# Optimization experiments

Measured on AMD Instinct MI355X. Metric: run time of the kernel, lower is better.

Reference implementation:

```python
import jax, jax.numpy as jnp
import numpy as np
from jax import lax

BS, K, N = 8, 8, 16            # batch, gathers per sample, picks per curve
T, WG = 3072, 64               # gather time samples, traces
H, WC = 256, 256               # CVEncoder ScaleSize
RH, RW = 1024, 512             # resize (also GatherEncoder outLen=RH)
T0, T1 = 0.0, 7000.0           # tInt[0], tInt[-1]


def setup_inputs() -> dict:
    key = jax.random.key(0)
    ks = jax.random.split(key, 8)
    gather = jax.random.normal(ks[0], (BS, K, T, WG), jnp.float32)
    # cv: times sorted, strictly > 0, within [T0, T1]; velocities within VMM range
    times = jnp.sort(jax.random.uniform(ks[1], (BS, K, N), minval=100.0, maxval=T1), axis=-1)
    vels = jnp.sort(jax.random.uniform(ks[2], (BS, K, N), minval=1500.0, maxval=4500.0), axis=-1)
    cv = jnp.stack([times, vels], axis=-1).astype(jnp.float32)
    VMM = jnp.tile(jnp.array([1500.0, 4500.0], jnp.float32), (BS, 1))
    def cw(k, shape):
        return (jax.random.normal(k, shape, jnp.float32) * 0.1)
    params = dict(
        w1=cw(ks[3], (1, 1, 3, 3)), b1=jnp.zeros((1,), jnp.float32), g1=jnp.ones((1,), jnp.float32), be1=jnp.zeros((1,), jnp.float32),
        w2=cw(ks[4], (2, 3, 3, 3)), b2=jnp.zeros((2,), jnp.float32), g2=jnp.ones((2,), jnp.float32), be2=jnp.zeros((2,), jnp.float32),
        w3=cw(ks[5], (1, 2, 3, 2)), b3=jnp.zeros((1,), jnp.float32), g3=jnp.ones((1,), jnp.float32), be3=jnp.zeros((1,), jnp.float32),
        wf=cw(ks[6], (1, 1, 3, 3)), bf=jnp.zeros((1,), jnp.float32), gf=jnp.ones((1,), jnp.float32), bef=jnp.zeros((1,), jnp.float32),
    )
    return {"gather": gather, "cv": cv, "VMM": VMM, **params}


def _conv(x, w, b, stride, pad):
    y = lax.conv_general_dilated(x, w, stride, pad, dimension_numbers=("NCHW", "OIHW", "NCHW"))
    return y + b[None, :, None, None]


def _bn(x, g, b, eps=1e-5):
    # training-mode BatchNorm2d: stats over (N, H, W)
    m = jnp.mean(x, (0, 2, 3), keepdims=True)
    v = jnp.var(x, (0, 2, 3), keepdims=True)
    return (x - m) / jnp.sqrt(v + eps) * g[None, :, None, None] + b[None, :, None, None]


def _lrelu(x):
    return jnp.where(x >= 0, x, 0.1 * x)


def _cbl(x, w, b, g, be, stride):
    return _lrelu(_bn(_conv(x, w, b, stride, "VALID"), g, be))


def _maxpool(x, k):
    p = k // 2
    return lax.reduce_window(x, -jnp.inf, lax.max, (1, 1, k, k), (1, 1, 1, 1),
                             ((0, 0), (0, 0), (p, p), (p, p)))


def _cv_mask(cv, VMM):
    # normalize times to fractional row index and velocities to fractional col index
    dt = (T1 - T0) / (H - 1)
    t_idx = (cv[..., 0] - T0) / dt                                        # (BS,K,N)
    dv = (VMM[:, 1] - VMM[:, 0]) / (WC - 1)                               # (BS,)
    v_idx = (cv[..., 1] - VMM[:, 0, None, None]) / dv[:, None, None]      # (BS,K,N)
    t_flat = t_idx.reshape(-1, N)
    v_flat = v_idx.reshape(-1, N)
    tq = jnp.arange(H, dtype=jnp.float32)
    # per-curve piecewise-linear interpolation of v over the time grid
    v_curve = jax.vmap(lambda xp, fp: jnp.interp(tq, xp, fp))(t_flat, v_flat)  # (M,H)
    v_int = jnp.clip(v_curve.astype(jnp.int32), 0, WC - 1)
    M = BS * K
    mask = jnp.full((M, H, WC), 0.01, jnp.float32)
    mask = mask.at[jnp.arange(M)[:, None], jnp.arange(H)[None, :], v_int].add(0.9)
    mask = mask.reshape(BS, K, H, WC)
    # bilinear resize, half-pixel centers == torch align_corners=False
    return jax.image.resize(mask, (BS, K, RH, RW), method="linear")


def _forward(gather, cv, VMM, w1, b1, g1, be1, w2, b2, g2, be2, w3, b3, g3, be3, wf, bf, gf, bef):
    cv_mask = lax.stop_gradient(_cv_mask(cv, VMM))          # CVEncoder runs under no_grad
    x = gather.reshape(-1, 1, T, WG)                        # (BS*K,1,T,WG)
    x = x / jnp.max(jnp.abs(x))                             # mode='mute': keep sign
    x = _cbl(x, w1, b1, g1, be1, (3, 2))                    # (M,1,1024,31)
    xcat = jnp.concatenate([x, _maxpool(x, 3), _maxpool(x, 5)], axis=1)
    x = _cbl(xcat, w2, b2, g2, be2, (3, 2))                 # (M,2,341,15)
    x = _cbl(x, w3, b3, g3, be3, (3, 2))                    # (M,1,113,7)
    x = jax.image.resize(x, (x.shape[0], 1, RH, 1), method="linear")
    genr = x.reshape(BS, K, RH, 1)
    mix = jnp.sum(genr * cv_mask, axis=1, keepdims=True)    # (BS,1,RH,RW)
    y = _conv(mix, wf, bf, (1, 1), ((1, 1), (1, 1)))
    return _lrelu(_bn(y, gf, bef))


def reference(gather, cv, VMM, w1, b1, g1, be1, w2, b2, g2, be2, w3, b3, g3, be3, wf, bf, gf, bef):
    return _forward(gather, cv, VMM, w1, b1, g1, be1, w2, b2, g2, be2, w3, b3, g3, be3, wf, bf, gf, bef)
```

## Files before the change

kernel.cpp:

```cpp
#include <hip/hip_runtime.h>
#include <math.h>

#define BSZ 8
#define KG  8
#define NP  16
#define MM  64
#define TT  3072
#define WGN 64
#define HH  256
#define WCN 256
#define RHN 1024
#define RWN 512

#define C1H 1024
#define C1W 31
#define C2H 341
#define C2W 15
#define C3H 113
#define C3W 7

#define N1 (MM*C1H*C1W)
#define N2 (MM*C2H*C2W)
#define N3 (MM*C3H*C3W)
#define NF (BSZ*RHN*RWN)

#define SL 64
__device__ __forceinline__ int stat_slot(int bid) {
    return ((bid & 7) << 3) | ((bid >> 3) & 7);
}

#define OFF_VINT 5376
#define OFF_Y1   (OFF_VINT + MM*HH*4)
#define OFF_Y2   (OFF_Y1  + N1*4)
#define OFF_Y3   (OFF_Y2  + 2*N2*4)
#define OFF_GENR (OFF_Y3  + N3*4)
#define OFF_Y5   (OFF_GENR + MM*RHN*4)

__device__ __forceinline__ void blockAdd2(double s, double ss, double* o0, double* o1) {
    __shared__ double red[4][2];
    __syncthreads();
    int lane = threadIdx.x & 63, wid = threadIdx.x >> 6;
#pragma unroll
    for (int off = 32; off > 0; off >>= 1) {
        s  += __shfl_down(s,  off, 64);
        ss += __shfl_down(ss, off, 64);
    }
    if (lane == 0) { red[wid][0] = s; red[wid][1] = ss; }
    __syncthreads();
    if (threadIdx.x == 0) {
        double a = 0, b = 0;
        int nw = blockDim.x >> 6;
        for (int i = 0; i < nw; i++) { a += red[i][0]; b += red[i][1]; }
        int slot = stat_slot(blockIdx.x);
        atomicAdd(&o0[slot], a); atomicAdd(&o1[slot], b);
    }
}

__device__ __forceinline__ float2 bn_ab(const double* __restrict__ sums, int c,
                                        const float* __restrict__ g,
                                        const float* __restrict__ be, double n) {
    double sum = 0, sumsq = 0;
#pragma unroll 8
    for (int j = 0; j < SL; j++) {
        sum   += sums[(2 * c) * SL + j];
        sumsq += sums[(2 * c + 1) * SL + j];
    }
    double mean = sum / n;
    double var  = sumsq / n - mean * mean;
    double a = (double)g[c] / sqrt(var + 1e-5);
    return make_float2((float)a, (float)((double)be[c] - mean * a));
}

#define K1_R 16
#define K1_ROWS (3*K1_R)
#define K1_CH 4
__global__ void k_conv1(const float* __restrict__ g, const float* __restrict__ w1,
                        const float* __restrict__ b1,
                        float* __restrict__ y1, double* sums) {
    __shared__ float sm[K1_ROWS * WGN];
    int m  = blockIdx.x >> 4;
    int bg = blockIdx.x & 15;
    const float4* src0 = (const float4*)(g + (size_t)m * TT * WGN
                                           + (size_t)(bg * K1_CH * K1_R * 3) * WGN);
    float w[9];
#pragma unroll
    for (int i = 0; i < 9; i++) w[i] = w1[i];
    float bb = b1[0];
    float4 ra0, ra1, ra2, rb0, rb1, rb2;
    ra0 = src0[threadIdx.x];
    ra1 = src0[threadIdx.x + 256];
    ra2 = src0[threadIdx.x + 512];
    double s = 0, ss = 0;
    float4* dst = (float4*)sm;
#pragma unroll
    for (int i = 0; i < K1_CH; i++) {
        if (i & 1) {
            dst[threadIdx.x]       = rb0;
            dst[threadIdx.x + 256] = rb1;
            dst[threadIdx.x + 512] = rb2;
        } else {
            dst[threadIdx.x]       = ra0;
            dst[threadIdx.x + 256] = ra1;
            dst[threadIdx.x + 512] = ra2;
        }
        __syncthreads();
        if (i + 1 < K1_CH) {
            const float4* srcn = src0 + (size_t)(i + 1) * 768;
            if (i & 1) {
                ra0 = srcn[threadIdx.x];
                ra1 = srcn[threadIdx.x + 256];
                ra2 = srcn[threadIdx.x + 512];
            } else {
                rb0 = srcn[threadIdx.x];
                rb1 = srcn[threadIdx.x + 256];
                rb2 = srcn[threadIdx.x + 512];
            }
        }
        int oh0 = (bg * K1_CH + i) * K1_R;
        float* yb = y1 + (size_t)m * C1H * C1W + (size_t)oh0 * C1W;
        for (int o = threadIdx.x; o < K1_R * C1W; o += 256) {
            int lo = o / C1W, ow = o % C1W;
            const float* xp = sm + (3 * lo) * WGN + ow * 2;
            float acc = bb;
#pragma unroll
            for (int r = 0; r < 3; r++)
#pragma unroll
                for (int c = 0; c < 3; c++) acc += w[r * 3 + c] * xp[r * WGN + c];
            yb[o] = acc;
            s += acc; ss += (double)acc * (double)acc;
        }
        __syncthreads();
    }
    blockAdd2(s, ss, &sums[0], &sums[SL]);
}

#define F2_OH 32
#define F2_NCH 11
#define F2_NRMAX (3*F2_OH + 4)
__global__ void k_fused2(const float* __restrict__ y1, const double* __restrict__ sums_r,
                         const float* __restrict__ g1, const float* __restrict__ be1,
                         const float* __restrict__ w2, const float* __restrict__ b2,
                         float* __restrict__ y2, double* sums) {
    __shared__ float sact[F2_NRMAX][32];
    __shared__ float sr3[F2_NRMAX][32];
    __shared__ float sr5[F2_NRMAX][32];
    float2 ab1 = bn_ab(sums_r, 0, g1, be1, (double)N1);
    int m   = blockIdx.x / F2_NCH;
    int ch  = blockIdx.x % F2_NCH;
    int oh0 = ch * F2_OH;
    int OHa = min(F2_OH, C2H - oh0);
    int NR  = 3 * OHa + 4;
    int gl0 = 3 * oh0 - 2;
    const float* yp = y1 + (size_t)m * C1H * C1W;
    for (int i = threadIdx.x; i < NR * C1W; i += blockDim.x) {
        int l = i / C1W, w = i % C1W;
        int gr = gl0 + l;
        float v = -INFINITY;
        if (gr >= 0 && gr < C1H) {
            v = ab1.x * yp[gr * C1W + w] + ab1.y;
            v = v >= 0.f ? v : 0.1f * v;
        }
        sact[l][w] = v;
    }
    __syncthreads();
    for (int i = threadIdx.x; i < NR * C1W; i += blockDim.x) {
        int l = i / C1W, w = i % C1W;
        int wl1 = max(w - 1, 0), wr1 = min(w + 1, C1W - 1);
        int wl2 = max(w - 2, 0), wr2 = min(w + 2, C1W - 1);
        float c  = sact[l][w];
        float m3 = fmaxf(fmaxf(sact[l][wl1], c), sact[l][wr1]);
        float m5 = fmaxf(fmaxf(m3, sact[l][wl2]), sact[l][wr2]);
        sr3[l][w] = m3;
        sr5[l][w] = m5;
    }
    __syncthreads();
    double s0 = 0, ss0 = 0, s1 = 0, ss1 = 0;
    for (int o = threadIdx.x; o < OHa * C2W; o += blockDim.x) {
        int lo = o / C2W, ow = o % C2W;
        float a0 = b2[0], acc1 = b2[1];
#pragma unroll
        for (int i = 0; i < 3; i++) {
            int l = 3 * lo + 2 + i;
#pragma unroll
            for (int j = 0; j < 3; j++) {
                int wc = 2 * ow + j;
                float v0 = sact[l][wc];
                float v1 = fmaxf(fmaxf(sr3[l - 1][wc], sr3[l][wc]), sr3[l + 1][wc]);
                float v2 = fmaxf(fmaxf(fmaxf(sr5[l - 2][wc], sr5[l - 1][wc]), sr5[l][wc]),
                                 fmaxf(sr5[l + 1][wc], sr5[l + 2][wc]));
                int ki = i * 3 + j;
                a0   += w2[ki] * v0 + w2[9 + ki] * v1 + w2[18 + ki] * v2;
                acc1 += w2[27 + ki] * v0 + w2[36 + ki] * v1 + w2[45 + ki] * v2;
            }
        }
        size_t ob = (size_t)m * (2 * C2H * C2W) + (size_t)(oh0 + lo) * C2W + ow;
        y2[ob] = a0;
        y2[ob + C2H * C2W] = acc1;
        s0 += a0; ss0 += (double)a0 * a0;
        s1 += acc1; ss1 += (double)acc1 * acc1;
    }
    blockAdd2(s0, ss0, &sums[2 * SL], &sums[3 * SL]);
    blockAdd2(s1, ss1, &sums[4 * SL], &sums[5 * SL]);
}

__global__ void k_conv3(const float* __restrict__ y2, const double* __restrict__ sums_r,
                        const float* __restrict__ g2, const float* __restrict__ be2,
                        const float* __restrict__ w3, const float* __restrict__ b3,
                        float* __restrict__ y3, double* sums) {
    float2 ab20 = bn_ab(sums_r + 2 * SL, 0, g2, be2, (double)N2);
    float2 ab21 = bn_ab(sums_r + 2 * SL, 1, g2, be2, (double)N2);
    double s = 0, ss = 0;
    int stride = gridDim.x * blockDim.x;
    for (int idx = blockIdx.x * blockDim.x + threadIdx.x; idx < N3; idx += stride) {
        int ow = idx % C3W;
        int t2 = idx / C3W;
        int oh = t2 % C3H;
        int m  = t2 / C3H;
        float acc = b3[0];
#pragma unroll
        for (int i = 0; i < 2; i++) {
            float aa = i ? ab21.x : ab20.x, bb = i ? ab21.y : ab20.y;
            const float* cp = y2 + (size_t)m * (2 * C2H * C2W) + (size_t)i * C2H * C2W
                              + (size_t)(oh * 3) * C2W + ow * 2;
#pragma unroll
            for (int r = 0; r < 3; r++)
#pragma unroll
                for (int c = 0; c < 2; c++) {
                    float v = aa * cp[r * C2W + c] + bb;
                    v = v >= 0.f ? v : 0.1f * v;
                    acc += w3[i * 6 + r * 2 + c] * v;
                }
        }
        y3[idx] = acc;
        s += acc; ss += (double)acc * acc;
    }
    blockAdd2(s, ss, &sums[6 * SL], &sums[7 * SL]);
}

__global__ void k_vintgenr(const float* __restrict__ cv, const float* __restrict__ VMM,
                           const float* __restrict__ y3, const double* __restrict__ sums_r,
                           const float* __restrict__ g3, const float* __restrict__ be3,
                           int* __restrict__ vint, float* __restrict__ genr) {
    __shared__ float tt[NP], vv[NP];
    __shared__ float tile[C3H * C3W];
    int m = blockIdx.x;
    int b = m >> 3;
    float2 ab3 = bn_ab(sums_r + 6 * SL, 0, g3, be3, (double)N3);
    if (threadIdx.x < NP) {
        int n = threadIdx.x;
        float t = cv[(m * NP + n) * 2 + 0];
        float v = cv[(m * NP + n) * 2 + 1];
        float dt = 7000.0f / 255.0f;
        tt[n] = t / dt;
        float vmin = VMM[b * 2], vmax = VMM[b * 2 + 1];
        float dv = (vmax - vmin) / 255.0f;
        vv[n] = (v - vmin) / dv;
    }
    for (int i = threadIdx.x; i < C3H * C3W; i += blockDim.x) {
        float v = ab3.x * y3[m * C3H * C3W + i] + ab3.y;
        tile[i] = v >= 0.f ? v : 0.1f * v;
    }
    __syncthreads();
    {
        int h = threadIdx.x;
        float x = (float)h;
        float val;
        if (x <= tt[0]) val = vv[0];
        else if (x >= tt[NP - 1]) val = vv[NP - 1];
        else {
            int i = 1;
            while (i < NP - 1 && tt[i] <= x) i++;
            float d = tt[i] - tt[i - 1];
            val = (d != 0.f) ? vv[i - 1] + (x - tt[i - 1]) / d * (vv[i] - vv[i - 1]) : vv[i];
        }
        int vi = (int)val;
        vint[m * HH + h] = max(0, min(WCN - 1, vi));
    }
    const float cw0 = 4.f / 37.f, cw1 = 5.f / 37.f, cw2 = 6.f / 37.f, cw3 = 7.f / 37.f;
    const float cw[7] = { cw0, cw1, cw2, cw3, cw2, cw1, cw0 };
    for (int i = threadIdx.x; i < RHN; i += blockDim.x) {
        float sh = (i + 0.5f) * (113.0f / 1024.0f) - 0.5f;
        float fl = floorf(sh);
        float fr = sh - fl;
        int i0 = (int)fl, i1 = i0 + 1;
        i0 = max(0, min(C3H - 1, i0));
        i1 = max(0, min(C3H - 1, i1));
        float acc = 0.f;
#pragma unroll
        for (int x = 0; x < 7; x++) {
            float v = (1.f - fr) * tile[i0 * C3W + x] + fr * tile[i1 * C3W + x];
            acc += cw[x] * v;
        }
        genr[m * RHN + i] = acc;
    }
}

#define MC_TH 16
__device__ __forceinline__ void build_mix_tile(const float* __restrict__ genr,
                                               const int* __restrict__ vint,
                                               int b, int h0,
                                               float (*tile)[RWN + 2], float* Grow) {
    for (int i = threadIdx.x; i < (MC_TH + 2) * (RWN + 2); i += blockDim.x)
        ((float*)tile)[i] = 0.f;
    if (threadIdx.x < MC_TH + 2) Grow[threadIdx.x] = 0.f;
    __syncthreads();
    if (threadIdx.x < (MC_TH + 2) * KG) {
        int r = threadIdx.x / KG, k = threadIdx.x % KG;
        int h = h0 - 1 + r;
        if (h >= 0 && h < RHN) {
            int m = b * KG + k;
            float g = genr[m * RHN + h];
            atomicAdd(&Grow[r], g);
            float sh = (h + 0.5f) * 0.25f - 0.5f;
            float fl = floorf(sh);
            float fh = sh - fl;
            int ih0 = (int)fl, ih1 = ih0 + 1;
            ih0 = max(0, min(HH - 1, ih0));
            ih1 = max(0, min(HH - 1, ih1));
            int vv[2] = { vint[m * HH + ih0], vint[m * HH + ih1] };
            float aa[2] = { 0.9f * g * (1.f - fh), 0.9f * g * fh };
#pragma unroll
            for (int t = 0; t < 2; t++) {
                int v = vv[t]; float A = aa[t];
                if (v == 0) {
                    atomicAdd(&tile[r][1 + 0], A);
                    atomicAdd(&tile[r][1 + 1], 0.75f * A);
                    atomicAdd(&tile[r][1 + 2], 0.25f * A);
                } else if (v == WCN - 1) {
                    atomicAdd(&tile[r][1 + 509], 0.25f * A);
                    atomicAdd(&tile[r][1 + 510], 0.75f * A);
                    atomicAdd(&tile[r][1 + 511], A);
                } else {
                    atomicAdd(&tile[r][1 + 2 * v - 1], 0.25f * A);
                    atomicAdd(&tile[r][1 + 2 * v],     0.75f * A);
                    atomicAdd(&tile[r][1 + 2 * v + 1], 0.75f * A);
                    atomicAdd(&tile[r][1 + 2 * v + 2], 0.25f * A);
                }
            }
        }
    }
    __syncthreads();
    for (int i = threadIdx.x; i < (MC_TH + 2) * RWN; i += blockDim.x) {
        int r = i / RWN, w = i % RWN;
        int h = h0 - 1 + r;
        if (h >= 0 && h < RHN) tile[r][w + 1] += 0.01f * Grow[r];
    }
    __syncthreads();
}

__global__ void k_mixA(const float* __restrict__ genr, const int* __restrict__ vint,
                       const float* __restrict__ wf, const float* __restrict__ bf,
                       float* __restrict__ y5, double* sums) {
    __shared__ float tile[MC_TH + 2][RWN + 2];
    __shared__ float Grow[MC_TH + 2];
    int b   = blockIdx.x / (RHN / MC_TH);
    int h0  = (blockIdx.x % (RHN / MC_TH)) * MC_TH;
    build_mix_tile(genr, vint, b, h0, tile, Grow);
    float w[9];
#pragma unroll
    for (int i = 0; i < 9; i++) w[i] = wf[i];
    float bb = bf[0];
    double s = 0, ss = 0;
    for (int o = threadIdx.x; o < MC_TH * RWN; o += blockDim.x) {
        int lr = o / RWN, x = o % RWN;
        float acc = bb;
#pragma unroll
        for (int dr = 0; dr < 3; dr++)
#pragma unroll
            for (int dc = 0; dc < 3; dc++)
                acc += w[dr * 3 + dc] * tile[lr + dr][x + dc];
        y5[((size_t)b * RHN + (h0 + lr)) * RWN + x] = acc;
        s += acc; ss += (double)acc * acc;
    }
    blockAdd2(s, ss, &sums[8 * SL], &sums[9 * SL]);
}

__global__ void k_bnf(const float* __restrict__ y5, const double* __restrict__ sums_r,
                      const float* __restrict__ gf, const float* __restrict__ bef,
                      float* __restrict__ out) {
    float2 abf = bn_ab(sums_r + 8 * SL, 0, gf, bef, (double)NF);
    int stride = gridDim.x * blockDim.x;
    const float4* src = (const float4*)y5;
    float4* dst = (float4*)out;
    for (int i = blockIdx.x * blockDim.x + threadIdx.x; i < NF / 4; i += stride) {
        float4 v = src[i];
        float a0 = abf.x * v.x + abf.y;
        float a1 = abf.x * v.y + abf.y;
        float a2 = abf.x * v.z + abf.y;
        float a3 = abf.x * v.w + abf.y;
        v.x = a0 >= 0.f ? a0 : 0.1f * a0;
        v.y = a1 >= 0.f ? a1 : 0.1f * a1;
        v.z = a2 >= 0.f ? a2 : 0.1f * a2;
        v.w = a3 >= 0.f ? a3 : 0.1f * a3;
        dst[i] = v;
    }
}

extern "C" void kernel_launch(void* const* d_in, const int* in_sizes, int n_in,
                              void* d_out, int out_size, void* d_ws, size_t ws_size,
                              hipStream_t stream) {
    const float* gather = (const float*)d_in[0];
    const float* cv     = (const float*)d_in[1];
    const float* VMM    = (const float*)d_in[2];
    const float* w1 = (const float*)d_in[3];
    const float* b1 = (const float*)d_in[4];
    const float* g1 = (const float*)d_in[5];
    const float* be1 = (const float*)d_in[6];
    const float* w2 = (const float*)d_in[7];
    const float* b2 = (const float*)d_in[8];
    const float* g2 = (const float*)d_in[9];
    const float* be2 = (const float*)d_in[10];
    const float* w3 = (const float*)d_in[11];
    const float* b3 = (const float*)d_in[12];
    const float* g3 = (const float*)d_in[13];
    const float* be3 = (const float*)d_in[14];
    const float* wf = (const float*)d_in[15];
    const float* bf = (const float*)d_in[16];
    const float* gf = (const float*)d_in[17];
    const float* bef = (const float*)d_in[18];
    float* out = (float*)d_out;

    char* ws = (char*)d_ws;
    double* sums = (double*)ws;
    int*   vint  = (int*)(ws + OFF_VINT);
    float* y1    = (float*)(ws + OFF_Y1);
    float* y2    = (float*)(ws + OFF_Y2);
    float* y3    = (float*)(ws + OFF_Y3);
    float* genr  = (float*)(ws + OFF_GENR);
    float* y5    = (float*)(ws + OFF_Y5);

    hipMemsetAsync(d_ws, 0, 10 * SL * 8, stream);

    k_conv1<<<MM * 16, 256, 0, stream>>>(gather, w1, b1, y1, sums);
    k_fused2<<<MM * F2_NCH, 256, 0, stream>>>(y1, sums, g1, be1, w2, b2, y2, sums);
    k_conv3<<<198, 256, 0, stream>>>(y2, sums, g2, be2, w3, b3, y3, sums);
    k_vintgenr<<<MM, 256, 0, stream>>>(cv, VMM, y3, sums, g3, be3, vint, genr);
    k_mixA<<<BSZ * (RHN / MC_TH), 256, 0, stream>>>(genr, vint, wf, bf, y5, sums);
    k_bnf<<<2048, 256, 0, stream>>>(y5, sums, gf, bef, out);
}
```

Measured before the change: 184.4 us.

## Fuse vint/genr stage into neighbors and replace atomic BN stats with partial stores

Removes the separate vint/genr kernel by computing velocity indices in spare conv1 blocks and recomputing the resized, normalized genr values inline when building the mix tile. BatchNorm statistics are now written as per-block partials and reduced by one wave in the consumer kernel, replacing slot atomics and the workspace memset. Grid sizes are fixed so each thread handles a fixed number of elements. This trades one launch and a memset for redundant genr recomputation across mix blocks.

```diff
diff --git a/kernel.cpp b/kernel.cpp
--- a/kernel.cpp
+++ b/kernel.cpp
@@ -24,19 +24,40 @@
 #define N3 (MM*C3H*C3W)
 #define NF (BSZ*RHN*RWN)
 
-#define SL 64
-__device__ __forceinline__ int stat_slot(int bid) {
-    return ((bid & 7) << 3) | ((bid >> 3) & 7);
-}
-
-#define OFF_VINT 5376
+#define G1 1024
+#define G2 704
+#define G3 256
+#define G5 512
+#define G6 512
+
+#define P1S   0
+#define P1SS  1024
+#define P2S0  2048
+#define P2SS0 2752
+#define P2S1  3456
+#define P2SS1 4160
+#define P3S   4864
+#define P3SS  5120
+#define PFS   5376
+#define PFSS  5888
+
+#define OFF_VINT 51200
 #define OFF_Y1   (OFF_VINT + MM*HH*4)
 #define OFF_Y2   (OFF_Y1  + N1*4)
 #define OFF_Y3   (OFF_Y2  + 2*N2*4)
-#define OFF_GENR (OFF_Y3  + N3*4)
-#define OFF_Y5   (OFF_GENR + MM*RHN*4)
-
-__device__ __forceinline__ void blockAdd2(double s, double ss, double* o0, double* o1) {
+#define OFF_Y5   (OFF_Y3  + N3*4)
+
+#define K1_R 16
+#define K1_ROWS (3*K1_R)
+#define K1_CH 4
+#define F2_OH 32
+#define F2_NCH 11
+#define F2_NRMAX (3*F2_OH + 4)
+#define MC_TH 16
+
+__device__ __forceinline__ void blockStore2(double s, double ss,
+                                            double* __restrict__ o0,
+                                            double* __restrict__ o1) {
     __shared__ double red[4][2];
     __syncthreads();
     int lane = threadIdx.x & 63, wid = threadIdx.x >> 6;
@@ -49,35 +70,42 @@
     __syncthreads();
     if (threadIdx.x == 0) {
         double a = 0, b = 0;
-        int nw = blockDim.x >> 6;
-        for (int i = 0; i < nw; i++) { a += red[i][0]; b += red[i][1]; }
-        int slot = stat_slot(blockIdx.x);
-        atomicAdd(&o0[slot], a); atomicAdd(&o1[slot], b);
-    }
-}
-
-__device__ __forceinline__ float2 bn_ab(const double* __restrict__ sums, int c,
-                                        const float* __restrict__ g,
-                                        const float* __restrict__ be, double n) {
-    double sum = 0, sumsq = 0;
-#pragma unroll 8
-    for (int j = 0; j < SL; j++) {
-        sum   += sums[(2 * c) * SL + j];
-        sumsq += sums[(2 * c + 1) * SL + j];
-    }
-    double mean = sum / n;
-    double var  = sumsq / n - mean * mean;
-    double a = (double)g[c] / sqrt(var + 1e-5);
-    return make_float2((float)a, (float)((double)be[c] - mean * a));
-}
-
-#define K1_R 16
-#define K1_ROWS (3*K1_R)
-#define K1_CH 4
-__global__ void k_conv1(const float* __restrict__ g, const float* __restrict__ w1,
+#pragma unroll
+        for (int i = 0; i < 4; i++) { a += red[i][0]; b += red[i][1]; }
+        o0[blockIdx.x] = a; o1[blockIdx.x] = b;
+    }
+}
+
+__device__ __forceinline__ void bn_fold(const double* __restrict__ ps,
+                                        const double* __restrict__ pss,
+                                        int npart, const float* __restrict__ g, int gc,
+                                        const float* __restrict__ be,
+                                        double n, float2* outsh, int wave) {
+    if ((threadIdx.x >> 6) == wave) {
+        int lane = threadIdx.x & 63;
+        double s = 0, ss = 0;
+        for (int i = lane; i < npart; i += 64) { s += ps[i]; ss += pss[i]; }
+#pragma unroll
+        for (int off = 32; off > 0; off >>= 1) {
+            s  += __shfl_down(s,  off, 64);
+            ss += __shfl_down(ss, off, 64);
+        }
+        if (lane == 0) {
+            double mean = s / n;
+            double var  = ss / n - mean * mean;
+            double a = (double)g[gc] / sqrt(var + 1e-5);
+            *outsh = make_float2((float)a, (float)((double)be[gc] - mean * a));
+        }
+    }
+}
+
+__global__ void k_conv1(const float* __restrict__ g, const float* __restrict__ cv,
+                        const float* __restrict__ VMM, const float* __restrict__ w1,
                         const float* __restrict__ b1,
-                        float* __restrict__ y1, double* sums) {
+                        float* __restrict__ y1, int* __restrict__ vint,
+                        double* __restrict__ sums) {
     __shared__ float sm[K1_ROWS * WGN];
+    __shared__ float tt[NP], vv[NP];
     int m  = blockIdx.x >> 4;
     int bg = blockIdx.x & 15;
     const float4* src0 = (const float4*)(g + (size_t)m * TT * WGN
@@ -131,20 +159,48 @@
         }
         __syncthreads();
     }
-    blockAdd2(s, ss, &sums[0], &sums[SL]);
-}
-
-#define F2_OH 32
-#define F2_NCH 11
-#define F2_NRMAX (3*F2_OH + 4)
+    if (blockIdx.x < MM) {
+        int mv = blockIdx.x;
+        int b = mv >> 3;
+        if (threadIdx.x < NP) {
+            int n = threadIdx.x;
+            float t = cv[(mv * NP + n) * 2 + 0];
+            float v = cv[(mv * NP + n) * 2 + 1];
+            float dt = 7000.0f / 255.0f;
+            tt[n] = t / dt;
+            float vmin = VMM[b * 2], vmax = VMM[b * 2 + 1];
+            float dv = (vmax - vmin) / 255.0f;
+            vv[n] = (v - vmin) / dv;
+        }
+        __syncthreads();
+        int h = threadIdx.x;
+        float x = (float)h;
+        float val;
+        if (x <= tt[0]) val = vv[0];
+        else if (x >= tt[NP - 1]) val = vv[NP - 1];
+        else {
+            int i = 1;
+            while (i < NP - 1 && tt[i] <= x) i++;
+            float d = tt[i] - tt[i - 1];
+            val = (d != 0.f) ? vv[i - 1] + (x - tt[i - 1]) / d * (vv[i] - vv[i - 1]) : vv[i];
+        }
+        int vi = (int)val;
+        vint[mv * HH + h] = max(0, min(WCN - 1, vi));
+    }
+    blockStore2(s, ss, &sums[P1S], &sums[P1SS]);
+}
+
 __global__ void k_fused2(const float* __restrict__ y1, const double* __restrict__ sums_r,
                          const float* __restrict__ g1, const float* __restrict__ be1,
                          const float* __restrict__ w2, const float* __restrict__ b2,
-                         float* __restrict__ y2, double* sums) {
+                         float* __restrict__ y2, double* __restrict__ sums) {
     __shared__ float sact[F2_NRMAX][32];
     __shared__ float sr3[F2_NRMAX][32];
     __shared__ float sr5[F2_NRMAX][32];
-    float2 ab1 = bn_ab(sums_r, 0, g1, be1, (double)N1);
+    __shared__ float2 absh;
+    bn_fold(&sums_r[P1S], &sums_r[P1SS], G1, g1, 0, be1, (double)N1, &absh, 0);
+    __syncthreads();
+    float2 ab1 = absh;
     int m   = blockIdx.x / F2_NCH;
     int ch  = blockIdx.x % F2_NCH;
     int oh0 = ch * F2_OH;
@@ -199,19 +255,22 @@
         s0 += a0; ss0 += (double)a0 * a0;
         s1 += acc1; ss1 += (double)acc1 * acc1;
     }
-    blockAdd2(s0, ss0, &sums[2 * SL], &sums[3 * SL]);
-    blockAdd2(s1, ss1, &sums[4 * SL], &sums[5 * SL]);
+    blockStore2(s0, ss0, &sums[P2S0], &sums[P2SS0]);
+    blockStore2(s1, ss1, &sums[P2S1], &sums[P2SS1]);
 }
 
 __global__ void k_conv3(const float* __restrict__ y2, const double* __restrict__ sums_r,
                         const float* __restrict__ g2, const float* __restrict__ be2,
                         const float* __restrict__ w3, const float* __restrict__ b3,
-                        float* __restrict__ y3, double* sums) {
-    float2 ab20 = bn_ab(sums_r + 2 * SL, 0, g2, be2, (double)N2);
-    float2 ab21 = bn_ab(sums_r + 2 * SL, 1, g2, be2, (double)N2);
+                        float* __restrict__ y3, double* __restrict__ sums) {
+    __shared__ float2 absh[2];
+    bn_fold(&sums_r[P2S0], &sums_r[P2SS0], G2, g2, 0, be2, (double)N2, &absh[0], 0);
+    bn_fold(&sums_r[P2S1], &sums_r[P2SS1], G2, g2, 1, be2, (double)N2, &absh[1], 1);
+    __syncthreads();
+    float2 ab20 = absh[0], ab21 = absh[1];
     double s = 0, ss = 0;
-    int stride = gridDim.x * blockDim.x;
-    for (int idx = blockIdx.x * blockDim.x + threadIdx.x; idx < N3; idx += stride) {
+    int idx = blockIdx.x * 256 + threadIdx.x;
+    if (idx < N3) {
         int ow = idx % C3W;
         int t2 = idx / C3W;
         int oh = t2 % C3H;
@@ -232,84 +291,51 @@
                 }
         }
         y3[idx] = acc;
-        s += acc; ss += (double)acc * acc;
-    }
-    blockAdd2(s, ss, &sums[6 * SL], &sums[7 * SL]);
-}
-
-__global__ void k_vintgenr(const float* __restrict__ cv, const float* __restrict__ VMM,
-                           const float* __restrict__ y3, const double* __restrict__ sums_r,
-                           const float* __restrict__ g3, const float* __restrict__ be3,
-                           int* __restrict__ vint, float* __restrict__ genr) {
-    __shared__ float tt[NP], vv[NP];
-    __shared__ float tile[C3H * C3W];
-    int m = blockIdx.x;
-    int b = m >> 3;
-    float2 ab3 = bn_ab(sums_r + 6 * SL, 0, g3, be3, (double)N3);
-    if (threadIdx.x < NP) {
-        int n = threadIdx.x;
-        float t = cv[(m * NP + n) * 2 + 0];
-        float v = cv[(m * NP + n) * 2 + 1];
-        float dt = 7000.0f / 255.0f;
-        tt[n] = t / dt;
-        float vmin = VMM[b * 2], vmax = VMM[b * 2 + 1];
-        float dv = (vmax - vmin) / 255.0f;
-        vv[n] = (v - vmin) / dv;
-    }
-    for (int i = threadIdx.x; i < C3H * C3W; i += blockDim.x) {
-        float v = ab3.x * y3[m * C3H * C3W + i] + ab3.y;
-        tile[i] = v >= 0.f ? v : 0.1f * v;
-    }
-    __syncthreads();
-    {
-        int h = threadIdx.x;
-        float x = (float)h;
-        float val;
-        if (x <= tt[0]) val = vv[0];
-        else if (x >= tt[NP - 1]) val = vv[NP - 1];
-        else {
-            int i = 1;
-            while (i < NP - 1 && tt[i] <= x) i++;
-            float d = tt[i] - tt[i - 1];
-            val = (d != 0.f) ? vv[i - 1] + (x - tt[i - 1]) / d * (vv[i] - vv[i - 1]) : vv[i];
-        }
-        int vi = (int)val;
-        vint[m * HH + h] = max(0, min(WCN - 1, vi));
-    }
-    const float cw0 = 4.f / 37.f, cw1 = 5.f / 37.f, cw2 = 6.f / 37.f, cw3 = 7.f / 37.f;
-    const float cw[7] = { cw0, cw1, cw2, cw3, cw2, cw1, cw0 };
-    for (int i = threadIdx.x; i < RHN; i += blockDim.x) {
-        float sh = (i + 0.5f) * (113.0f / 1024.0f) - 0.5f;
-        float fl = floorf(sh);
-        float fr = sh - fl;
-        int i0 = (int)fl, i1 = i0 + 1;
-        i0 = max(0, min(C3H - 1, i0));
-        i1 = max(0, min(C3H - 1, i1));
-        float acc = 0.f;
-#pragma unroll
-        for (int x = 0; x < 7; x++) {
-            float v = (1.f - fr) * tile[i0 * C3W + x] + fr * tile[i1 * C3W + x];
-            acc += cw[x] * v;
-        }
-        genr[m * RHN + i] = acc;
-    }
-}
-
-#define MC_TH 16
-__device__ __forceinline__ void build_mix_tile(const float* __restrict__ genr,
-                                               const int* __restrict__ vint,
-                                               int b, int h0,
-                                               float (*tile)[RWN + 2], float* Grow) {
-    for (int i = threadIdx.x; i < (MC_TH + 2) * (RWN + 2); i += blockDim.x)
+        s = acc; ss = (double)acc * acc;
+    }
+    blockStore2(s, ss, &sums[P3S], &sums[P3SS]);
+}
+
+__global__ void k_mixA(const float* __restrict__ y3, const int* __restrict__ vint,
+                       const double* __restrict__ sums_r,
+                       const float* __restrict__ g3, const float* __restrict__ be3,
+                       const float* __restrict__ wf, const float* __restrict__ bf,
+                       float* __restrict__ y5, double* __restrict__ sums) {
+    __shared__ float tile[MC_TH + 2][RWN + 2];
+    __shared__ float Grow[MC_TH + 2];
+    __shared__ float2 absh;
+    bn_fold(&sums_r[P3S], &sums_r[P3SS], G3, g3, 0, be3, (double)N3, &absh, 0);
+    int b   = blockIdx.x / (RHN / MC_TH);
+    int h0  = (blockIdx.x % (RHN / MC_TH)) * MC_TH;
+    for (int i = threadIdx.x; i < (MC_TH + 2) * (RWN + 2); i += 256)
         ((float*)tile)[i] = 0.f;
     if (threadIdx.x < MC_TH + 2) Grow[threadIdx.x] = 0.f;
     __syncthreads();
+    float2 ab3 = absh;
     if (threadIdx.x < (MC_TH + 2) * KG) {
         int r = threadIdx.x / KG, k = threadIdx.x % KG;
         int h = h0 - 1 + r;
         if (h >= 0 && h < RHN) {
             int m = b * KG + k;
-            float g = genr[m * RHN + h];
+            const float cw0 = 4.f / 37.f, cw1 = 5.f / 37.f, cw2 = 6.f / 37.f, cw3 = 7.f / 37.f;
+            const float cw[7] = { cw0, cw1, cw2, cw3, cw2, cw1, cw0 };
+            float shg = (h + 0.5f) * (113.0f / 1024.0f) - 0.5f;
+            float flg = floorf(shg);
+            float frg = shg - flg;
+            int gi0 = (int)flg, gi1 = gi0 + 1;
+            gi0 = max(0, min(C3H - 1, gi0));
+            gi1 = max(0, min(C3H - 1, gi1));
+            const float* yp0 = y3 + (size_t)m * (C3H * C3W) + gi0 * C3W;
+            const float* yp1 = y3 + (size_t)m * (C3H * C3W) + gi1 * C3W;
+            float g = 0.f;
+#pragma unroll
+            for (int x = 0; x < 7; x++) {
+                float t0 = ab3.x * yp0[x] + ab3.y;
+                t0 = t0 >= 0.f ? t0 : 0.1f * t0;
+                float t1 = ab3.x * yp1[x] + ab3.y;
+                t1 = t1 >= 0.f ? t1 : 0.1f * t1;
+                g += cw[x] * ((1.f - frg) * t0 + frg * t1);
+            }
             atomicAdd(&Grow[r], g);
             float sh = (h + 0.5f) * 0.25f - 0.5f;
             float fl = floorf(sh);
@@ -317,11 +343,11 @@
             int ih0 = (int)fl, ih1 = ih0 + 1;
             ih0 = max(0, min(HH - 1, ih0));
             ih1 = max(0, min(HH - 1, ih1));
-            int vv[2] = { vint[m * HH + ih0], vint[m * HH + ih1] };
+            int vv2[2] = { vint[m * HH + ih0], vint[m * HH + ih1] };
             float aa[2] = { 0.9f * g * (1.f - fh), 0.9f * g * fh };
 #pragma unroll
             for (int t = 0; t < 2; t++) {
-                int v = vv[t]; float A = aa[t];
+                int v = vv2[t]; float A = aa[t];
                 if (v == 0) {
                     atomicAdd(&tile[r][1 + 0], A);
                     atomicAdd(&tile[r][1 + 1], 0.75f * A);
@@ -340,29 +366,19 @@
         }
     }
     __syncthreads();
-    for (int i = threadIdx.x; i < (MC_TH + 2) * RWN; i += blockDim.x) {
+    for (int i = threadIdx.x; i < (MC_TH + 2) * RWN; i += 256) {
         int r = i / RWN, w = i % RWN;
         int h = h0 - 1 + r;
         if (h >= 0 && h < RHN) tile[r][w + 1] += 0.01f * Grow[r];
     }
     __syncthreads();
-}
-
-__global__ void k_mixA(const float* __restrict__ genr, const int* __restrict__ vint,
-                       const float* __restrict__ wf, const float* __restrict__ bf,
-                       float* __restrict__ y5, double* sums) {
-    __shared__ float tile[MC_TH + 2][RWN + 2];
-    __shared__ float Grow[MC_TH + 2];
-    int b   = blockIdx.x / (RHN / MC_TH);
-    int h0  = (blockIdx.x % (RHN / MC_TH)) * MC_TH;
-    build_mix_tile(genr, vint, b, h0, tile, Grow);
     float w[9];
 #pragma unroll
     for (int i = 0; i < 9; i++) w[i] = wf[i];
     float bb = bf[0];
     double s = 0, ss = 0;
-    for (int o = threadIdx.x; o < MC_TH * RWN; o += blockDim.x) {
-        int lr = o / RWN, x = o % RWN;
+    for (int o = threadIdx.x; o < MC_TH * RWN; o += 256) {
+        int lr = o >> 9, x = o & (RWN - 1);
         float acc = bb;
 #pragma unroll
         for (int dr = 0; dr < 3; dr++)
@@ -372,17 +388,22 @@
         y5[((size_t)b * RHN + (h0 + lr)) * RWN + x] = acc;
         s += acc; ss += (double)acc * acc;
     }
-    blockAdd2(s, ss, &sums[8 * SL], &sums[9 * SL]);
+    blockStore2(s, ss, &sums[PFS], &sums[PFSS]);
 }
 
 __global__ void k_bnf(const float* __restrict__ y5, const double* __restrict__ sums_r,
                       const float* __restrict__ gf, const float* __restrict__ bef,
                       float* __restrict__ out) {
-    float2 abf = bn_ab(sums_r + 8 * SL, 0, gf, bef, (double)NF);
-    int stride = gridDim.x * blockDim.x;
+    __shared__ float2 absh;
+    bn_fold(&sums_r[PFS], &sums_r[PFSS], G5, gf, 0, bef, (double)NF, &absh, 0);
+    __syncthreads();
+    float2 abf = absh;
     const float4* src = (const float4*)y5;
     float4* dst = (float4*)out;
-    for (int i = blockIdx.x * blockDim.x + threadIdx.x; i < NF / 4; i += stride) {
+    int base = blockIdx.x * 256 + threadIdx.x;
+#pragma unroll
+    for (int j = 0; j < 8; j++) {
+        int i = base + j * (G6 * 256);
         float4 v = src[i];
         float a0 = abf.x * v.x + abf.y;
         float a1 = abf.x * v.y + abf.y;
@@ -426,15 +447,11 @@
     float* y1    = (float*)(ws + OFF_Y1);
     float* y2    = (float*)(ws + OFF_Y2);
     float* y3    = (float*)(ws + OFF_Y3);
-    float* genr  = (float*)(ws + OFF_GENR);
     float* y5    = (float*)(ws + OFF_Y5);
 
-    hipMemsetAsync(d_ws, 0, 10 * SL * 8, stream);
-
-    k_conv1<<<MM * 16, 256, 0, stream>>>(gather, w1, b1, y1, sums);
-    k_fused2<<<MM * F2_NCH, 256, 0, stream>>>(y1, sums, g1, be1, w2, b2, y2, sums);
-    k_conv3<<<198, 256, 0, stream>>>(y2, sums, g2, be2, w3, b3, y3, sums);
-    k_vintgenr<<<MM, 256, 0, stream>>>(cv, VMM, y3, sums, g3, be3, vint, genr);
-    k_mixA<<<BSZ * (RHN / MC_TH), 256, 0, stream>>>(genr, vint, wf, bf, y5, sums);
-    k_bnf<<<2048, 256, 0, stream>>>(y5, sums, gf, bef, out);
-}
+    k_conv1<<<G1, 256, 0, stream>>>(gather, cv, VMM, w1, b1, y1, vint, sums);
+    k_fused2<<<G2, 256, 0, stream>>>(y1, sums, g1, be1, w2, b2, y2, sums);
+    k_conv3<<<G3, 256, 0, stream>>>(y2, sums, g2, be2, w3, b3, y3, sums);
+    k_mixA<<<G5, 256, 0, stream>>>(y3, vint, sums, g3, be3, wf, bf, y5, sums);
+    k_bnf<<<G6, 256, 0, stream>>>(y5, sums, gf, bef, out);
+}
```

Result: faster. 174.7 us (-5.2%).
